# Optimization experiments

Measured on AMD Instinct MI355X. Metric: run time of the kernel, lower is better.

Reference implementation:

```python
import jax, jax.numpy as jnp
import numpy as np

B, M, DM = 8, 1024, 1024
H, DH, R = 16, 64, 32
DFF, R1, R2, RO = 4096, 512, 512, 512
EPS = 1e-12


def layernorm(x, g, b):
    mu = jnp.mean(x, axis=-1, keepdims=True)
    var = jnp.mean(jnp.square(x - mu), axis=-1, keepdims=True)
    return (x - mu) * jax.lax.rsqrt(var + EPS) * g + b


def setup_inputs() -> dict:
    key = jax.random.key(0)
    ks = jax.random.split(key, 24)
    s = lambda *sh: 1.0 / np.sqrt(sh[-2] if len(sh) > 1 else sh[-1])
    d = {}
    d['x'] = jax.random.normal(ks[0], (B, M, DM), jnp.float32)
    d['mask'] = jnp.zeros((B, M), jnp.float32)  # additive attention mask
    # per-head low-rank QKV factors: P:(H,DM,R), V:(H,R,DH), b:(H,DH)
    for i, nm in enumerate(['q', 'k', 'v']):
        d['P' + nm] = jax.random.normal(ks[1 + 3 * i], (H, DM, R), jnp.float32) * 0.02
        d['V' + nm] = jax.random.normal(ks[2 + 3 * i], (H, R, DH), jnp.float32) * 0.02
        d['b' + nm] = jnp.zeros((H, DH), jnp.float32)
    # attention output projection (low-rank) + LN1
    d['Uo'] = jax.random.normal(ks[10], (DM, RO), jnp.float32) * 0.02
    d['Vo'] = jax.random.normal(ks[11], (RO, DM), jnp.float32) * 0.02
    d['bo_attn'] = jnp.zeros((DM,), jnp.float32)
    d['g1'] = jnp.ones((DM,), jnp.float32)
    d['beta1'] = jnp.zeros((DM,), jnp.float32)
    # FFN low-rank factors + LN2
    d['U1'] = jax.random.normal(ks[12], (DM, R1), jnp.float32) * 0.02
    d['V1'] = jax.random.normal(ks[13], (R1, DFF), jnp.float32) * 0.02
    d['b1'] = jnp.zeros((DFF,), jnp.float32)
    d['U2'] = jax.random.normal(ks[14], (DFF, R2), jnp.float32) * 0.02
    d['V2'] = jax.random.normal(ks[15], (R2, DM), jnp.float32) * 0.02
    d['b2'] = jnp.zeros((DM,), jnp.float32)
    d['g2'] = jnp.ones((DM,), jnp.float32)
    d['beta2'] = jnp.zeros((DM,), jnp.float32)
    return d


def reference(x, mask, Pq, Vq, bq, Pk, Vk, bk, Pv, Vv, bv,
              Uo, Vo, bo_attn, g1, beta1,
              U1, V1, b1, U2, V2, b2, g2, beta2):
    # low-rank Q/K/V: x @ P -> (B,H,M,R), then @ V -> (B,H,M,DH), + bias
    def qkv(P, V, b):
        tmp = jnp.einsum('bmd,hdr->bhmr', x, P)
        return jnp.einsum('bhmr,hre->bhme', tmp, V) + b[None, :, None, :]

    Q = qkv(Pq, Vq, bq)
    K = qkv(Pk, Vk, bk)
    V = qkv(Pv, Vv, bv)
    scale = 1.0 / jnp.sqrt(jnp.asarray(DH, x.dtype))
    scores = jnp.einsum('bhme,bhne->bhmn', Q, K) * scale
    scores = scores + mask[:, None, None, :]  # additive mask broadcast over heads/queries
    probs = jax.nn.softmax(scores, axis=-1)
    attn = jnp.einsum('bhmn,bhne->bhme', probs, V)  # (B,H,M,DH)
    attn = attn.transpose(0, 2, 1, 3).reshape(attn.shape[0], attn.shape[2], -1)  # (B,M,DM)
    x1 = layernorm(x + (attn @ Uo) @ Vo + bo_attn, g1, beta1)
    # FFN: GELU((x1 @ U1) @ V1 + b1) @ U2 @ V2 + b2 (flashsvd_ffn semantics)
    mid = x1 @ U1
    hidden = jax.nn.gelu(mid @ V1 + b1, approximate=False)
    y = (hidden @ U2) @ V2 + b2
    return layernorm(x1 + y, g2, beta2)
```

## Files before the change

### kernel.cpp

```cpp
#include <hip/hip_runtime.h>
#include <hip/hip_bf16.h>
#include <math.h>

typedef unsigned short u16;
typedef unsigned int u32;
typedef __attribute__((ext_vector_type(8))) short bf16x8;
typedef __attribute__((ext_vector_type(4))) float f32x4;
typedef __attribute__((ext_vector_type(2))) unsigned int u32x2;
typedef __attribute__((ext_vector_type(4))) unsigned int u32x4;

#define B_ 8
#define M_ 1024
#define DM_ 1024
#define H_ 16
#define DH_ 64
#define NR_ 8192

__device__ __forceinline__ u16 f2bf(float f) {
    unsigned u = __float_as_uint(f);
    u += 0x7FFFu + ((u >> 16) & 1u);
    return (u16)(u >> 16);
}

__device__ __forceinline__ void gload16(const void* g, void* l) {
    __builtin_amdgcn_global_load_lds(
        (const __attribute__((address_space(1))) void*)g,
        (__attribute__((address_space(3))) void*)l, 16, 0, 0);
}

__device__ __forceinline__ u32 lds_addr(const void* p) {
    return (u32)(uintptr_t)(const __attribute__((address_space(3))) void*)p;
}

__device__ void conv_dev(const float* __restrict__ in, u16* __restrict__ out,
                         int bid, int tid) {
#pragma unroll
    for (int j = 0; j < 4; ++j) {
        int i = bid * 4096 + j * 1024 + tid * 4;
        float4 v = *reinterpret_cast<const float4*>(in + i);
        unsigned long long p = (unsigned long long)f2bf(v.x)
                             | ((unsigned long long)f2bf(v.y) << 16)
                             | ((unsigned long long)f2bf(v.z) << 32)
                             | ((unsigned long long)f2bf(v.w) << 48);
        *reinterpret_cast<unsigned long long*>(out + i) = p;
    }
}

__device__ void prep_p_dev(const float* __restrict__ P, u16* __restrict__ Pt,
                           int h, int kc, int tid, float* sm) {
    float (*Ps)[33] = (float(*)[33])sm;
#pragma unroll
    for (int i = 0; i < 16; ++i) {
        int e = tid + i * 256;
        int kk = e >> 5, r = e & 31;
        Ps[kk][r] = P[(size_t)h * 32768 + (size_t)(kc + kk) * 32 + r];
    }
    __syncthreads();
#pragma unroll
    for (int i = 0; i < 16; ++i) {
        int e = tid + i * 256;
        int r = e >> 7, k = e & 127;
        Pt[(size_t)(h * 32 + r) * 1024 + kc + k] = f2bf(Ps[k][r]);
    }
}

__device__ void prep_f_dev(const float* __restrict__ V, u16* __restrict__ Ft,
                           int h, int tid, float* sm) {
    float (*Vs)[65] = (float(*)[65])sm;
#pragma unroll
    for (int i = 0; i < 8; ++i) {
        int e = tid + i * 256;
        int r = e >> 6, c = e & 63;
        Vs[r][c] = V[(size_t)h * 2048 + r * 64 + c];
    }
    __syncthreads();
#pragma unroll
    for (int i = 0; i < 8; ++i) {
        int idx = tid + i * 256;
        int e = idx >> 5, r = idx & 31;
        Ft[(size_t)h * 2560 + e * 40 + r] = f2bf(Vs[r][e]);
    }
}

__device__ void transp_dev(const float* __restrict__ in, u16* __restrict__ out,
                           int R, int C, int bx, int by, int tid, float* sm) {
    float (*t)[65] = (float(*)[65])sm;
    const int rb = by * 64, cb = bx * 64;
#pragma unroll
    for (int i = 0; i < 16; ++i) {
        int e = tid + i * 256;
        int r = e >> 6, c = e & 63;
        t[r][c] = in[(size_t)(rb + r) * C + cb + c];
    }
    __syncthreads();
#pragma unroll
    for (int i = 0; i < 16; ++i) {
        int e = tid + i * 256;
        int r = e >> 6, c = e & 63;
        out[(size_t)(cb + r) * R + rb + c] = f2bf(t[c][r]);
    }
}

__global__ __launch_bounds__(256) void prep_all(
    const float* __restrict__ x,
    const float* __restrict__ Pq, const float* __restrict__ Pk, const float* __restrict__ Pv,
    const float* __restrict__ Vq, const float* __restrict__ Vk, const float* __restrict__ Vv,
    const float* __restrict__ Uo, const float* __restrict__ Vo,
    const float* __restrict__ U1, const float* __restrict__ V1,
    const float* __restrict__ U2, const float* __restrict__ V2,
    u16* __restrict__ Xb, u16* __restrict__ Pt,
    u16* __restrict__ Ftq, u16* __restrict__ Ftk, u16* __restrict__ Ftv,
    u16* __restrict__ Uot, u16* __restrict__ Vot,
    u16* __restrict__ U1t, u16* __restrict__ V1t,
    u16* __restrict__ U2t, u16* __restrict__ V2t) {
    __shared__ float smem[4224];
    const int bid = blockIdx.x, tid = threadIdx.x;
    if (bid < 2048) {
        conv_dev(x, Xb, bid, tid);
    } else if (bid < 2432) {
        int t = bid - 2048, which = t >> 7, tt = t & 127;
        const float* P = which == 0 ? Pq : (which == 1 ? Pk : Pv);
        prep_p_dev(P, Pt + (size_t)which * 524288, tt >> 3, (tt & 7) * 128, tid, smem);
    } else if (bid < 2480) {
        int t = bid - 2432, which = t >> 4;
        const float* V = which == 0 ? Vq : (which == 1 ? Vk : Vv);
        u16* F = which == 0 ? Ftq : (which == 1 ? Ftk : Ftv);
        prep_f_dev(V, F, t & 15, tid, smem);
    } else if (bid < 2608) {
        int t = bid - 2480;
        transp_dev(Uo, Uot, 1024, 512, t & 7, t >> 3, tid, smem);
    } else if (bid < 2736) {
        int t = bid - 2608;
        transp_dev(Vo, Vot, 512, 1024, t & 15, t >> 4, tid, smem);
    } else if (bid < 2864) {
        int t = bid - 2736;
        transp_dev(U1, U1t, 1024, 512, t & 7, t >> 3, tid, smem);
    } else if (bid < 3376) {
        int t = bid - 2864;
        transp_dev(V1, V1t, 512, 4096, t & 63, t >> 6, tid, smem);
    } else if (bid < 3888) {
        int t = bid - 3376;
        transp_dev(U2, U2t, 4096, 512, t & 7, t >> 3, tid, smem);
    } else {
        int t = bid - 3888;
        transp_dev(V2, V2t, 512, 1024, t & 15, t >> 4, tid, smem);
    }
}

template <int EPI, int NF>
__global__ __launch_bounds__(256) void gemm_bf16(const u16* __restrict__ A,
                                                 const u16* __restrict__ Bt,
                                                 const float* __restrict__ bias,
                                                 void* __restrict__ Cout,
                                                 int K, int N) {
    constexpr int BN = NF * 32;
    __shared__ u16 As[128 * 64];
    __shared__ u16 Bs[BN * 64];
    const int tid = threadIdx.x;
    const int lane = tid & 63, wv = tid >> 6;

    const int NX = gridDim.x;
    const int flat = blockIdx.x + blockIdx.y * NX;
    const int q = (NX * gridDim.y) >> 3;
    const int nid = (flat & 7) * q + (flat >> 3);
    const int row0 = (nid / NX) * 128, col0 = (nid % NX) * BN;

    const int frow = lane & 15, fk8 = lane >> 4;
    const int wm = (wv >> 1) * 64, wn = (wv & 1) * (BN / 2);

    f32x4 acc[4][NF];
    const f32x4 z4 = {0.f, 0.f, 0.f, 0.f};
#pragma unroll
    for (int i = 0; i < 4; ++i)
#pragma unroll
        for (int j = 0; j < NF; ++j) acc[i][j] = z4;

    for (int k0 = 0; k0 < K; k0 += 64) {
#pragma unroll
        for (int i = 0; i < 4; ++i) {
            int rr = (i * 4 + wv) * 8 + (lane >> 3);
            int cc = ((lane & 7) ^ (rr & 7)) * 8;
            gload16(A + (size_t)(row0 + rr) * K + k0 + cc,
                    (char*)As + (i * 4 + wv) * 1024);
        }
#pragma unroll
        for (int i = 0; i < NF; ++i) {
            int rr = (i * 4 + wv) * 8 + (lane >> 3);
            int cc = ((lane & 7) ^ (rr & 7)) * 8;
            gload16(Bt + (size_t)(col0 + rr) * K + k0 + cc,
                    (char*)Bs + (i * 4 + wv) * 1024);
        }
        asm volatile("s_waitcnt vmcnt(0)" ::: "memory");
        __syncthreads();
#pragma unroll
        for (int kf = 0; kf < 2; ++kf) {
            bf16x8 af[4], bfr[NF];
#pragma unroll
            for (int mf = 0; mf < 4; ++mf) {
                int r = wm + mf * 16 + frow;
                int c16 = (kf * 4 + fk8) ^ (r & 7);
                af[mf] = *reinterpret_cast<const bf16x8*>((char*)As + r * 128 + c16 * 16);
            }
#pragma unroll
            for (int nf = 0; nf < NF; ++nf) {
                int r = wn + nf * 16 + frow;
                int c16 = (kf * 4 + fk8) ^ (r & 7);
                bfr[nf] = *reinterpret_cast<const bf16x8*>((char*)Bs + r * 128 + c16 * 16);
            }
#pragma unroll
            for (int mf = 0; mf < 4; ++mf)
#pragma unroll
                for (int nf = 0; nf < NF; ++nf)
                    acc[mf][nf] = __builtin_amdgcn_mfma_f32_16x16x32_bf16(
                        af[mf], bfr[nf], acc[mf][nf], 0, 0, 0);
        }
        __syncthreads();
    }

    const int orow = fk8 * 4, ocol = frow;
#pragma unroll
    for (int mf = 0; mf < 4; ++mf)
#pragma unroll
        for (int nf = 0; nf < NF; ++nf)
#pragma unroll
            for (int j = 0; j < 4; ++j) {
                int row = row0 + wm + mf * 16 + orow + j;
                int col = col0 + wn + nf * 16 + ocol;
                float v = acc[mf][nf][j];
                if (EPI == 2) {
                    v += bias[col];
                    v = 0.5f * v * (1.f + erff(v * 0.70710678118f));
                    ((u16*)Cout)[(size_t)row * N + col] = f2bf(v);
                } else if (EPI == 3) {
                    ((float*)Cout)[(size_t)row * N + col] = v;
                } else {
                    ((u16*)Cout)[(size_t)row * N + col] = f2bf(v);
                }
            }
}

__global__ __launch_bounds__(256) void gemm_qkv(const u16* __restrict__ A,
                                                const u16* __restrict__ Bt,
                                                const u16* __restrict__ Ftq,
                                                const u16* __restrict__ Ftk,
                                                const u16* __restrict__ Ftv,
                                                const float* __restrict__ bq,
                                                const float* __restrict__ bk,
                                                const float* __restrict__ bv,
                                                u16* __restrict__ Qo,
                                                u16* __restrict__ Ko,
                                                u16* __restrict__ Vo) {
    const int K = 1024;
    __shared__ u16 As[128 * 64];
    __shared__ u16 Bs[128 * 64];
    const int tid = threadIdx.x;
    const int lane = tid & 63, wv = tid >> 6;

    const int NX = gridDim.x;
    const int flat = blockIdx.x + blockIdx.y * NX;
    const int q = (NX * gridDim.y) >> 3;
    const int nid = (flat & 7) * q + (flat >> 3);
    const int row0 = (nid / NX) * 128, col0 = (nid % NX) * 128;

    const int frow = lane & 15, fk8 = lane >> 4;
    const int wm = (wv >> 1) * 64, wn = (wv & 1) * 64;

    f32x4 acc[4][4];
    const f32x4 z4 = {0.f, 0.f, 0.f, 0.f};
#pragma unroll
    for (int i = 0; i < 4; ++i)
#pragma unroll
        for (int j = 0; j < 4; ++j) acc[i][j] = z4;

    for (int k0 = 0; k0 < K; k0 += 64) {
#pragma unroll
        for (int i = 0; i < 4; ++i) {
            int rr = (i * 4 + wv) * 8 + (lane >> 3);
            int cc = ((lane & 7) ^ (rr & 7)) * 8;
            gload16(A + (size_t)(row0 + rr) * K + k0 + cc,
                    (char*)As + (i * 4 + wv) * 1024);
            gload16(Bt + (size_t)(col0 + rr) * K + k0 + cc,
                    (char*)Bs + (i * 4 + wv) * 1024);
        }
        asm volatile("s_waitcnt vmcnt(0)" ::: "memory");
        __syncthreads();
#pragma unroll
        for (int kf = 0; kf < 2; ++kf) {
            bf16x8 af[4], bfr[4];
#pragma unroll
            for (int mf = 0; mf < 4; ++mf) {
                int r = wm + mf * 16 + frow;
                int c16 = (kf * 4 + fk8) ^ (r & 7);
                af[mf] = *reinterpret_cast<const bf16x8*>((char*)As + r * 128 + c16 * 16);
            }
#pragma unroll
            for (int nf = 0; nf < 4; ++nf) {
                int r = wn + nf * 16 + frow;
                int c16 = (kf * 4 + fk8) ^ (r & 7);
                bfr[nf] = *reinterpret_cast<const bf16x8*>((char*)Bs + r * 128 + c16 * 16);
            }
#pragma unroll
            for (int mf = 0; mf < 4; ++mf)
#pragma unroll
                for (int nf = 0; nf < 4; ++nf)
                    acc[mf][nf] = __builtin_amdgcn_mfma_f32_16x16x32_bf16(
                        af[mf], bfr[nf], acc[mf][nf], 0, 0, 0);
        }
        __syncthreads();
    }

    u16* preg = (wv < 2) ? As + wv * 4096 : Bs + (wv - 2) * 4096;
#pragma unroll
    for (int mf = 0; mf < 4; ++mf)
#pragma unroll
        for (int nf = 0; nf < 4; ++nf)
#pragma unroll
            for (int j = 0; j < 4; ++j) {
                int r = mf * 16 + fk8 * 4 + j;
                int c = nf * 16 + frow;
                int byte = r * 128 + (((c >> 3) ^ (r & 7)) * 16) + (c & 7) * 2;
                *(u16*)((char*)preg + byte) = f2bf(acc[mf][nf][j]);
            }
    __syncthreads();

    const int f = col0 >> 9;
    const u16* Ft = f == 0 ? Ftq : (f == 1 ? Ftk : Ftv);
    const float* bias = f == 0 ? bq : (f == 1 ? bk : bv);
    u16* outp = f == 0 ? Qo : (f == 1 ? Ko : Vo);
    const int h0 = (((col0 & 511) + wn) >> 5);

#pragma unroll
    for (int hh = 0; hh < 2; ++hh) {
        const int h = h0 + hh;
        const u16* ftb = Ft + (size_t)h * 2560;
        bf16x8 bf2[4];
#pragma unroll
        for (int ef = 0; ef < 4; ++ef) {
            int e = ef * 16 + frow;
            bf2[ef] = *reinterpret_cast<const bf16x8*>(ftb + e * 40 + fk8 * 8);
        }
#pragma unroll
        for (int mf = 0; mf < 4; ++mf) {
            int r = mf * 16 + frow;
            bf16x8 af = *reinterpret_cast<const bf16x8*>(
                (char*)preg + r * 128 + (((hh * 4 + fk8) ^ (r & 7)) * 16));
#pragma unroll
            for (int ef = 0; ef < 4; ++ef) {
                f32x4 o = __builtin_amdgcn_mfma_f32_16x16x32_bf16(af, bf2[ef], z4, 0, 0, 0);
                int e = ef * 16 + frow;
                float bv_ = bias[h * 64 + e];
#pragma unroll
                for (int j = 0; j < 4; ++j) {
                    int row = row0 + wm + mf * 16 + fk8 * 4 + j;
                    int bb = row >> 10, m = row & 1023;
                    outp[(((size_t)(bb * 16 + h) << 10) + m) * 64 + e] = f2bf(o[j] + bv_);
                }
            }
        }
    }
}

__global__ __launch_bounds__(256) void gemm_db(const u16* __restrict__ A,
                                               const u16* __restrict__ Bt,
                                               u16* __restrict__ Cout,
                                               int K, int N) {
    __shared__ u16 As[2][128 * 64];
    __shared__ u16 Bs[2][64 * 64];
    const int tid = threadIdx.x;
    const int lane = tid & 63, wv = tid >> 6;

    const int NX = gridDim.x;
    const int flat = blockIdx.x + blockIdx.y * NX;
    const int q = (NX * gridDim.y) >> 3;
    const int nid = (flat & 7) * q + (flat >> 3);
    const int row0 = (nid / NX) * 128, col0 = (nid % NX) * 64;

    const int frow = lane & 15, fk8 = lane >> 4;
    const int wm = (wv >> 1) * 64, wn = (wv & 1) * 32;

    f32x4 acc[4][2];
    const f32x4 z4 = {0.f, 0.f, 0.f, 0.f};
#pragma unroll
    for (int i = 0; i < 4; ++i) {
        acc[i][0] = z4;
        acc[i][1] = z4;
    }

    const int srr = (lane >> 3);
    const int scc = (lane & 7);

#pragma unroll
    for (int i = 0; i < 4; ++i) {
        int rr = (i * 4 + wv) * 8 + srr;
        int cc = (scc ^ (rr & 7)) * 8;
        gload16(A + (size_t)(row0 + rr) * K + cc, (char*)&As[0][0] + (i * 4 + wv) * 1024);
    }
#pragma unroll
    for (int i = 0; i < 2; ++i) {
        int rr = (i * 4 + wv) * 8 + srr;
        int cc = (scc ^ (rr & 7)) * 8;
        gload16(Bt + (size_t)(col0 + rr) * K + cc, (char*)&Bs[0][0] + (i * 4 + wv) * 1024);
    }

    int cur = 0;
    for (int k0 = 0; k0 < K; k0 += 64) {
        __syncthreads();
        if (k0 + 64 < K) {
            int kn = k0 + 64;
#pragma unroll
            for (int i = 0; i < 4; ++i) {
                int rr = (i * 4 + wv) * 8 + srr;
                int cc = (scc ^ (rr & 7)) * 8;
                gload16(A + (size_t)(row0 + rr) * K + kn + cc,
                        (char*)&As[cur ^ 1][0] + (i * 4 + wv) * 1024);
            }
#pragma unroll
            for (int i = 0; i < 2; ++i) {
                int rr = (i * 4 + wv) * 8 + srr;
                int cc = (scc ^ (rr & 7)) * 8;
                gload16(Bt + (size_t)(col0 + rr) * K + kn + cc,
                        (char*)&Bs[cur ^ 1][0] + (i * 4 + wv) * 1024);
            }
        }
#pragma unroll
        for (int kf = 0; kf < 2; ++kf) {
            bf16x8 af[4], bfr[2];
#pragma unroll
            for (int mf = 0; mf < 4; ++mf) {
                int r = wm + mf * 16 + frow;
                int c16 = (kf * 4 + fk8) ^ (r & 7);
                af[mf] = *reinterpret_cast<const bf16x8*>((char*)&As[cur][0] + r * 128 + c16 * 16);
            }
#pragma unroll
            for (int nf = 0; nf < 2; ++nf) {
                int r = wn + nf * 16 + frow;
                int c16 = (kf * 4 + fk8) ^ (r & 7);
                bfr[nf] = *reinterpret_cast<const bf16x8*>((char*)&Bs[cur][0] + r * 128 + c16 * 16);
            }
#pragma unroll
            for (int mf = 0; mf < 4; ++mf)
#pragma unroll
                for (int nf = 0; nf < 2; ++nf)
                    acc[mf][nf] = __builtin_amdgcn_mfma_f32_16x16x32_bf16(
                        af[mf], bfr[nf], acc[mf][nf], 0, 0, 0);
        }
        cur ^= 1;
    }

#pragma unroll
    for (int mf = 0; mf < 4; ++mf)
#pragma unroll
        for (int nf = 0; nf < 2; ++nf)
#pragma unroll
            for (int j = 0; j < 4; ++j) {
                int row = row0 + wm + mf * 16 + fk8 * 4 + j;
                int col = col0 + wn + nf * 16 + frow;
                Cout[(size_t)row * N + col] = f2bf(acc[mf][nf][j]);
            }
}

__global__ __launch_bounds__(256) void attn_mfma(const u16* __restrict__ Q,
                                                 const u16* __restrict__ K,
                                                 const u16* __restrict__ V,
                                                 const float* __restrict__ mask,
                                                 u16* __restrict__ O) {
    __shared__ u16 Ks[2][4096];
    __shared__ u16 Vt[2][4096];
    __shared__ u16 Pw[4096];
    const int flat = blockIdx.x;
    const int nid = (flat & 7) * 256 + (flat >> 3);
    const int hb = nid >> 4, qt = nid & 15;
    const int b = hb >> 4, h = hb & 15;
    const int tid = threadIdx.x, lane = tid & 63, wv = tid >> 6;
    const int frow = lane & 15, fk8 = lane >> 4;
    const size_t base = (size_t)hb * 65536;
    const float LOG2E = 1.44269504089f;
    const int srr = lane >> 3, scc = lane & 7;

    int voff[2];
#pragma unroll
    for (int i = 0; i < 2; ++i) {
        int c = (i * 4 + wv) * 64 + lane;
        int kb = c >> 5, db = (c >> 3) & 3, kr = (c >> 1) & 3, hf = c & 1;
        voff[i] = (kb * 4 + kr) * 64 + db * 16 + hf * 8;
    }

#pragma unroll
    for (int i = 0; i < 2; ++i) {
        int rr = (i * 4 + wv) * 8 + srr;
        int cc = (scc ^ (rr & 7)) * 8;
        gload16(Q + base + (size_t)(qt * 64 + rr) * 64 + cc,
                (char*)Pw + (i * 4 + wv) * 1024);
        gload16(K + base + (size_t)rr * 64 + cc,
                (char*)&Ks[0][0] + (i * 4 + wv) * 1024);
    }
#pragma unroll
    for (int i = 0; i < 2; ++i)
        gload16(V + base + voff[i], (char*)&Vt[0][0] + (i * 4 + wv) * 1024);
    asm volatile("s_waitcnt vmcnt(0)" ::: "memory");
    __syncthreads();

    bf16x8 qfrag[2];
#pragma unroll
    for (int kf = 0; kf < 2; ++kf) {
        int qr = wv * 16 + frow;
        int c16 = (kf * 4 + fk8) ^ (qr & 7);
        qfrag[kf] = *reinterpret_cast<const bf16x8*>((char*)Pw + qr * 128 + c16 * 16);
    }

    u32 vta[4];
    {
        u32 vt0 = lds_addr(&Vt[0][0]) + fk8 * 1024 + frow * 2;
#pragma unroll
        for (int nf = 0; nf < 4; ++nf) vta[nf] = vt0 + nf * 128;
    }

    char* pwW = (char*)Pw + wv * 2048 + frow * 128 + (fk8 & 1) * 8;
    char* pwR = (char*)Pw + wv * 2048 + frow * 128;
    const float* mrow = mask + b * M_;

    float m_i = -1e30f, l_i = 0.f;
    const f32x4 z4 = {0.f, 0.f, 0.f, 0.f};
    f32x4 o_acc[4] = {z4, z4, z4, z4};

    int cur = 0;
    for (int kt = 0; kt < 16; ++kt) {
        if (kt < 15) {
            const int nxt = cur ^ 1;
#pragma unroll
            for (int i = 0; i < 2; ++i) {
                int rr = (i * 4 + wv) * 8 + srr;
                int cc = (scc ^ (rr & 7)) * 8;
                gload16(K + base + (kt + 1) * 4096 + (size_t)rr * 64 + cc,
                        (char*)&Ks[nxt][0] + (i * 4 + wv) * 1024);
            }
#pragma unroll
            for (int i = 0; i < 2; ++i)
                gload16(V + base + (kt + 1) * 4096 + voff[i],
                        (char*)&Vt[nxt][0] + (i * 4 + wv) * 1024);
        }

        const char* ksb = (char*)&Ks[cur][0];
        const u32 vbo = (u32)(cur * 8192);

        f32x4 sacc[4] = {z4, z4, z4, z4};
        __builtin_amdgcn_s_setprio(1);
#pragma unroll
        for (int kf = 0; kf < 2; ++kf)
#pragma unroll
            for (int nf = 0; nf < 4; ++nf) {
                int kr = nf * 16 + frow;
                int c16 = (kf * 4 + fk8) ^ (kr & 7);
                bf16x8 ak = *reinterpret_cast<const bf16x8*>(ksb + kr * 128 + c16 * 16);
                sacc[nf] = __builtin_amdgcn_mfma_f32_16x16x32_bf16(ak, qfrag[kf], sacc[nf], 0, 0, 0);
            }
        __builtin_amdgcn_s_setprio(0);

        float tval[4][4];
        float tmax = -1e30f;
#pragma unroll
        for (int nf = 0; nf < 4; ++nf) {
            float4 mk = *reinterpret_cast<const float4*>(mrow + kt * 64 + nf * 16 + fk8 * 4);
            float t0 = fmaf(sacc[nf][0], 0.125f, mk.x);
            float t1 = fmaf(sacc[nf][1], 0.125f, mk.y);
            float t2 = fmaf(sacc[nf][2], 0.125f, mk.z);
            float t3 = fmaf(sacc[nf][3], 0.125f, mk.w);
            tval[nf][0] = t0; tval[nf][1] = t1; tval[nf][2] = t2; tval[nf][3] = t3;
            tmax = fmaxf(tmax, fmaxf(fmaxf(t0, t1), fmaxf(t2, t3)));
        }
        tmax = fmaxf(tmax, __shfl_xor(tmax, 16));
        tmax = fmaxf(tmax, __shfl_xor(tmax, 32));

        if (__any(tmax > m_i + 8.f)) {
            float mnew = fmaxf(m_i, tmax);
            float c = exp2f((m_i - mnew) * LOG2E);
            m_i = mnew;
            l_i *= c;
#pragma unroll
            for (int j = 0; j < 4; ++j) {
                float cj = __shfl(c, fk8 * 4 + j);
#pragma unroll
                for (int nf = 0; nf < 4; ++nf) o_acc[nf][j] *= cj;
            }
        }

        const float ml = m_i * LOG2E;
        float rs = 0.f;
#pragma unroll
        for (int nf = 0; nf < 4; ++nf) {
            float p0 = exp2f(fmaf(tval[nf][0], LOG2E, -ml));
            float p1 = exp2f(fmaf(tval[nf][1], LOG2E, -ml));
            float p2 = exp2f(fmaf(tval[nf][2], LOG2E, -ml));
            float p3 = exp2f(fmaf(tval[nf][3], LOG2E, -ml));
            rs += (p0 + p1) + (p2 + p3);
            u32 w0 = __builtin_amdgcn_perm(__float_as_uint(p1), __float_as_uint(p0), 0x07060302u);
            u32 w1 = __builtin_amdgcn_perm(__float_as_uint(p3), __float_as_uint(p2), 0x07060302u);
            u32x2 wp = {w0, w1};
            *reinterpret_cast<u32x2*>(pwW + (((nf * 2 + (fk8 >> 1)) ^ (frow & 7)) * 16)) = wp;
        }
        rs += __shfl_xor(rs, 16);
        rs += __shfl_xor(rs, 32);
        l_i += rs;

#pragma unroll
        for (int kf = 0; kf < 2; ++kf) {
            bf16x8 ap = *reinterpret_cast<const bf16x8*>(pwR + (((kf * 4 + fk8) ^ (frow & 7)) * 16));
            u32 a0 = vta[0] + vbo, a1 = vta[1] + vbo, a2 = vta[2] + vbo, a3 = vta[3] + vbo;
            u32x2 r0, r1, r2, r3, r4, r5, r6, r7;
            if (kf == 0) {
                asm volatile("ds_read_b64_tr_b16 %0, %1" : "=&v"(r0) : "v"(a0));
                asm volatile("ds_read_b64_tr_b16 %0, %1 offset:512" : "=&v"(r1) : "v"(a0));
                asm volatile("ds_read_b64_tr_b16 %0, %1" : "=&v"(r2) : "v"(a1));
                asm volatile("ds_read_b64_tr_b16 %0, %1 offset:512" : "=&v"(r3) : "v"(a1));
                asm volatile("ds_read_b64_tr_b16 %0, %1" : "=&v"(r4) : "v"(a2));
                asm volatile("ds_read_b64_tr_b16 %0, %1 offset:512" : "=&v"(r5) : "v"(a2));
                asm volatile("ds_read_b64_tr_b16 %0, %1" : "=&v"(r6) : "v"(a3));
                asm volatile("ds_read_b64_tr_b16 %0, %1 offset:512" : "=&v"(r7) : "v"(a3));
            } else {
                asm volatile("ds_read_b64_tr_b16 %0, %1 offset:4096" : "=&v"(r0) : "v"(a0));
                asm volatile("ds_read_b64_tr_b16 %0, %1 offset:4608" : "=&v"(r1) : "v"(a0));
                asm volatile("ds_read_b64_tr_b16 %0, %1 offset:4096" : "=&v"(r2) : "v"(a1));
                asm volatile("ds_read_b64_tr_b16 %0, %1 offset:4608" : "=&v"(r3) : "v"(a1));
                asm volatile("ds_read_b64_tr_b16 %0, %1 offset:4096" : "=&v"(r4) : "v"(a2));
                asm volatile("ds_read_b64_tr_b16 %0, %1 offset:4608" : "=&v"(r5) : "v"(a2));
                asm volatile("ds_read_b64_tr_b16 %0, %1 offset:4096" : "=&v"(r6) : "v"(a3));
                asm volatile("ds_read_b64_tr_b16 %0, %1 offset:4608" : "=&v"(r7) : "v"(a3));
            }
            asm volatile("s_waitcnt lgkmcnt(0)" ::: "memory");
            __builtin_amdgcn_sched_barrier(0);
            __builtin_amdgcn_s_setprio(1);
            {
                u32x4 vv = {r0.x, r0.y, r1.x, r1.y};
                bf16x8 fb; __builtin_memcpy(&fb, &vv, 16);
                o_acc[0] = __builtin_amdgcn_mfma_f32_16x16x32_bf16(ap, fb, o_acc[0], 0, 0, 0);
            }
            {
                u32x4 vv = {r2.x, r2.y, r3.x, r3.y};
                bf16x8 fb; __builtin_memcpy(&fb, &vv, 16);
                o_acc[1] = __builtin_amdgcn_mfma_f32_16x16x32_bf16(ap, fb, o_acc[1], 0, 0, 0);
            }
            {
                u32x4 vv = {r4.x, r4.y, r5.x, r5.y};
                bf16x8 fb; __builtin_memcpy(&fb, &vv, 16);
                o_acc[2] = __builtin_amdgcn_mfma_f32_16x16x32_bf16(ap, fb, o_acc[2], 0, 0, 0);
            }
            {
                u32x4 vv = {r6.x, r6.y, r7.x, r7.y};
                bf16x8 fb; __builtin_memcpy(&fb, &vv, 16);
                o_acc[3] = __builtin_amdgcn_mfma_f32_16x16x32_bf16(ap, fb, o_acc[3], 0, 0, 0);
            }
            __builtin_amdgcn_s_setprio(0);
        }

        asm volatile("s_waitcnt vmcnt(0)" ::: "memory");
        __syncthreads();
        cur ^= 1;
    }

#pragma unroll
    for (int j = 0; j < 4; ++j) {
        float lq = __shfl(l_i, fk8 * 4 + j);
        float inv = 1.f / lq;
        int grow = qt * 64 + wv * 16 + fk8 * 4 + j;
        size_t obase = ((size_t)(b * M_ + grow)) * DM_ + h * 64;
#pragma unroll
        for (int nf = 0; nf < 4; ++nf)
            O[obase + nf * 16 + frow] = f2bf(o_acc[nf][j] * inv);
    }
}

template <bool WBF>
__global__ __launch_bounds__(256) void ln_kernel(const float* __restrict__ y,
                                                 const float* __restrict__ res,
                                                 const float* __restrict__ bias,
                                                 const float* __restrict__ g,
                                                 const float* __restrict__ beta,
                                                 float* __restrict__ outf,
                                                 u16* __restrict__ outb) {
    __shared__ float red[2][4];
    const int row = blockIdx.x, tid = threadIdx.x;
    const size_t base = (size_t)row * 1024 + tid * 4;
    float4 v = *reinterpret_cast<const float4*>(y + base);
    float4 r = *reinterpret_cast<const float4*>(res + base);
    float4 bb = *reinterpret_cast<const float4*>(bias + tid * 4);
    v.x += r.x + bb.x; v.y += r.y + bb.y; v.z += r.z + bb.z; v.w += r.w + bb.w;
    float sum = v.x + v.y + v.z + v.w;
    float sq = v.x * v.x + v.y * v.y + v.z * v.z + v.w * v.w;
#pragma unroll
    for (int off = 32; off; off >>= 1) {
        sum += __shfl_down(sum, off);
        sq += __shfl_down(sq, off);
    }
    if ((tid & 63) == 0) { red[0][tid >> 6] = sum; red[1][tid >> 6] = sq; }
    __syncthreads();
    sum = red[0][0] + red[0][1] + red[0][2] + red[0][3];
    sq = red[1][0] + red[1][1] + red[1][2] + red[1][3];
    float mu = sum * (1.f / 1024.f);
    float var = sq * (1.f / 1024.f) - mu * mu;
    float rstd = rsqrtf(var + 1e-12f);
    float4 gg = *reinterpret_cast<const float4*>(g + tid * 4);
    float4 be = *reinterpret_cast<const float4*>(beta + tid * 4);
    float4 o;
    o.x = (v.x - mu) * rstd * gg.x + be.x;
    o.y = (v.y - mu) * rstd * gg.y + be.y;
    o.z = (v.z - mu) * rstd * gg.z + be.z;
    o.w = (v.w - mu) * rstd * gg.w + be.w;
    *reinterpret_cast<float4*>(outf + base) = o;
    if (WBF) {
        unsigned long long p = (unsigned long long)f2bf(o.x)
                             | ((unsigned long long)f2bf(o.y) << 16)
                             | ((unsigned long long)f2bf(o.z) << 32)
                             | ((unsigned long long)f2bf(o.w) << 48);
        *reinterpret_cast<unsigned long long*>(outb + base) = p;
    }
}

extern "C" void kernel_launch(void* const* d_in, const int* in_sizes, int n_in,
                              void* d_out, int out_size, void* d_ws, size_t ws_size,
                              hipStream_t stream) {
    const float* x    = (const float*)d_in[0];
    const float* mask = (const float*)d_in[1];
    const float* Pq   = (const float*)d_in[2];
    const float* Vq   = (const float*)d_in[3];
    const float* bq   = (const float*)d_in[4];
    const float* Pk   = (const float*)d_in[5];
    const float* Vk   = (const float*)d_in[6];
    const float* bk   = (const float*)d_in[7];
    const float* Pv   = (const float*)d_in[8];
    const float* Vv   = (const float*)d_in[9];
    const float* bv   = (const float*)d_in[10];
    const float* Uo   = (const float*)d_in[11];
    const float* Vo   = (const float*)d_in[12];
    const float* bo   = (const float*)d_in[13];
    const float* g1   = (const float*)d_in[14];
    const float* be1  = (const float*)d_in[15];
    const float* U1   = (const float*)d_in[16];
    const float* V1   = (const float*)d_in[17];
    const float* b1   = (const float*)d_in[18];
    const float* U2   = (const float*)d_in[19];
    const float* V2   = (const float*)d_in[20];
    const float* b2   = (const float*)d_in[21];
    const float* g2   = (const float*)d_in[22];
    const float* be2  = (const float*)d_in[23];
    float* out = (float*)d_out;

    const size_t MB = 1048576;
    char* ws = (char*)d_ws;
    u16* Pt  = (u16*)(ws + 0);
    u16* Ftq = (u16*)(ws + 3 * MB);
    u16* Ftk = (u16*)(ws + 3 * MB + 131072);
    u16* Ftv = (u16*)(ws + 3 * MB + 262144);
    u16* Uot = (u16*)(ws + 4 * MB);
    u16* Vot = (u16*)(ws + 5 * MB);
    u16* U1t = (u16*)(ws + 6 * MB);
    u16* V1t = (u16*)(ws + 7 * MB);
    u16* U2t = (u16*)(ws + 11 * MB);
    u16* V2t = (u16*)(ws + 15 * MB);
    u16* Xb  = (u16*)(ws + 16 * MB);
    u16* Qb  = (u16*)(ws + 56 * MB);
    u16* Kb  = (u16*)(ws + 72 * MB);
    u16* Vb  = (u16*)(ws + 88 * MB);
    u16* Ob  = (u16*)(ws + 104 * MB);
    u16* Hb  = (u16*)(ws + 32 * MB);
    float* Yf = (float*)(ws + 56 * MB);
    u16* Tb  = (u16*)(ws + 96 * MB);
    float* X1f = (float*)(ws + 120 * MB);

    prep_all<<<4016, 256, 0, stream>>>(x, Pq, Pk, Pv, Vq, Vk, Vv,
                                       Uo, Vo, U1, V1, U2, V2,
                                       Xb, Pt, Ftq, Ftk, Ftv,
                                       Uot, Vot, U1t, V1t, U2t, V2t);

    gemm_qkv<<<dim3(12, 64), 256, 0, stream>>>(Xb, Pt, Ftq, Ftk, Ftv,
                                               bq, bk, bv, Qb, Kb, Vb);

    attn_mfma<<<2048, 256, 0, stream>>>(Qb, Kb, Vb, mask, Ob);

    gemm_db<<<dim3(8, 64), 256, 0, stream>>>(Ob, Uot, Tb, 1024, 512);
    gemm_bf16<3, 4><<<dim3(8, 64), 256, 0, stream>>>(Tb, Vot, nullptr, Yf, 512, 1024);
    ln_kernel<true><<<8192, 256, 0, stream>>>(Yf, x, bo, g1, be1, X1f, Xb);

    gemm_db<<<dim3(8, 64), 256, 0, stream>>>(Xb, U1t, Tb, 1024, 512);
    gemm_bf16<2, 4><<<dim3(32, 64), 256, 0, stream>>>(Tb, V1t, b1, Hb, 512, 4096);
    gemm_db<<<dim3(8, 64), 256, 0, stream>>>(Hb, U2t, Tb, 4096, 512);
    gemm_bf16<3, 4><<<dim3(8, 64), 256, 0, stream>>>(Tb, V2t, nullptr, Yf, 512, 1024);
    ln_kernel<false><<<8192, 256, 0, stream>>>(Yf, X1f, b2, g2, be2, out, nullptr);
}
```

Baseline: 335.5 us.

## Keep P in registers, single-buffer K, pad V tile to raise attention occupancy

The attention kernel stops staging softmax probabilities through LDS. It packs the bf16 P values directly into MFMA A-operand registers by permuting the V key order to match. K becomes single-buffered, V is padded to avoid bank conflicts, Q is staged in the V buffer, and launch bounds ask for 8 blocks per CU. The intent is less LDS traffic and footprint so more blocks fit per CU. The cost is an extra barrier per iteration and less overlap between the K prefetch and compute.

```diff
diff --git a/kernel.cpp b/kernel.cpp
--- a/kernel.cpp
+++ b/kernel.cpp
@@ -459,14 +459,13 @@
             }
 }
 
-__global__ __launch_bounds__(256) void attn_mfma(const u16* __restrict__ Q,
-                                                 const u16* __restrict__ K,
-                                                 const u16* __restrict__ V,
-                                                 const float* __restrict__ mask,
-                                                 u16* __restrict__ O) {
-    __shared__ u16 Ks[2][4096];
-    __shared__ u16 Vt[2][4096];
-    __shared__ u16 Pw[4096];
+__global__ __launch_bounds__(256, 8) void attn_mfma(const u16* __restrict__ Q,
+                                                    const u16* __restrict__ K,
+                                                    const u16* __restrict__ V,
+                                                    const float* __restrict__ mask,
+                                                    u16* __restrict__ O) {
+    __shared__ u16 Ks[4096];
+    __shared__ u16 Vt[8448];
     const int flat = blockIdx.x;
     const int nid = (flat & 7) * 256 + (flat >> 3);
     const int hb = nid >> 4, qt = nid & 15;
@@ -480,9 +479,10 @@
     int voff[2];
 #pragma unroll
     for (int i = 0; i < 2; ++i) {
-        int c = (i * 4 + wv) * 64 + lane;
-        int kb = c >> 5, db = (c >> 3) & 3, kr = (c >> 1) & 3, hf = c & 1;
-        voff[i] = (kb * 4 + kr) * 64 + db * 16 + hf * 8;
+        int r = i * 4 + wv;
+        int keyp = (2 * (r >> 2) + (lane >> 5)) * 16 + (r & 3) * 4 + ((lane >> 1) & 3);
+        int d = ((lane >> 3) & 3) * 16 + (lane & 1) * 8;
+        voff[i] = keyp * 64 + d;
     }
 
 #pragma unroll
@@ -490,33 +490,31 @@
         int rr = (i * 4 + wv) * 8 + srr;
         int cc = (scc ^ (rr & 7)) * 8;
         gload16(Q + base + (size_t)(qt * 64 + rr) * 64 + cc,
-                (char*)Pw + (i * 4 + wv) * 1024);
-        gload16(K + base + (size_t)rr * 64 + cc,
-                (char*)&Ks[0][0] + (i * 4 + wv) * 1024);
-    }
-#pragma unroll
-    for (int i = 0; i < 2; ++i)
-        gload16(V + base + voff[i], (char*)&Vt[0][0] + (i * 4 + wv) * 1024);
+                (char*)Vt + (i * 4 + wv) * 1024);
+    }
     asm volatile("s_waitcnt vmcnt(0)" ::: "memory");
     __syncthreads();
-
     bf16x8 qfrag[2];
 #pragma unroll
     for (int kf = 0; kf < 2; ++kf) {
         int qr = wv * 16 + frow;
         int c16 = (kf * 4 + fk8) ^ (qr & 7);
-        qfrag[kf] = *reinterpret_cast<const bf16x8*>((char*)Pw + qr * 128 + c16 * 16);
-    }
-
-    u32 vta[4];
-    {
-        u32 vt0 = lds_addr(&Vt[0][0]) + fk8 * 1024 + frow * 2;
-#pragma unroll
-        for (int nf = 0; nf < 4; ++nf) vta[nf] = vt0 + nf * 128;
-    }
-
-    char* pwW = (char*)Pw + wv * 2048 + frow * 128 + (fk8 & 1) * 8;
-    char* pwR = (char*)Pw + wv * 2048 + frow * 128;
+        qfrag[kf] = *reinterpret_cast<const bf16x8*>((char*)Vt + qr * 128 + c16 * 16);
+    }
+    __syncthreads();
+#pragma unroll
+    for (int i = 0; i < 2; ++i) {
+        int rr = (i * 4 + wv) * 8 + srr;
+        int cc = (scc ^ (rr & 7)) * 8;
+        gload16(K + base + (size_t)rr * 64 + cc, (char*)Ks + (i * 4 + wv) * 1024);
+    }
+#pragma unroll
+    for (int i = 0; i < 2; ++i)
+        gload16(V + base + voff[i], (char*)Vt + (i * 4 + wv) * 1056);
+    asm volatile("s_waitcnt vmcnt(0)" ::: "memory");
+    __syncthreads();
+
+    const u32 plbase = lds_addr(Vt) + fk8 * 1056 + frow * 2;
     const float* mrow = mask + b * M_;
 
     float m_i = -1e30f, l_i = 0.f;
@@ -525,6 +523,20 @@
 
     int cur = 0;
     for (int kt = 0; kt < 16; ++kt) {
+        f32x4 sacc[4] = {z4, z4, z4, z4};
+        __builtin_amdgcn_s_setprio(1);
+#pragma unroll
+        for (int kf = 0; kf < 2; ++kf)
+#pragma unroll
+            for (int nf = 0; nf < 4; ++nf) {
+                int kr = nf * 16 + frow;
+                int c16 = (kf * 4 + fk8) ^ (kr & 7);
+                bf16x8 ak = *reinterpret_cast<const bf16x8*>((char*)Ks + kr * 128 + c16 * 16);
+                sacc[nf] = __builtin_amdgcn_mfma_f32_16x16x32_bf16(ak, qfrag[kf], sacc[nf], 0, 0, 0);
+            }
+        __builtin_amdgcn_s_setprio(0);
+        __syncthreads();
+
         if (kt < 15) {
             const int nxt = cur ^ 1;
 #pragma unroll
@@ -532,29 +544,13 @@
                 int rr = (i * 4 + wv) * 8 + srr;
                 int cc = (scc ^ (rr & 7)) * 8;
                 gload16(K + base + (kt + 1) * 4096 + (size_t)rr * 64 + cc,
-                        (char*)&Ks[nxt][0] + (i * 4 + wv) * 1024);
+                        (char*)Ks + (i * 4 + wv) * 1024);
             }
 #pragma unroll
             for (int i = 0; i < 2; ++i)
                 gload16(V + base + (kt + 1) * 4096 + voff[i],
-                        (char*)&Vt[nxt][0] + (i * 4 + wv) * 1024);
-        }
-
-        const char* ksb = (char*)&Ks[cur][0];
-        const u32 vbo = (u32)(cur * 8192);
-
-        f32x4 sacc[4] = {z4, z4, z4, z4};
-        __builtin_amdgcn_s_setprio(1);
-#pragma unroll
-        for (int kf = 0; kf < 2; ++kf)
-#pragma unroll
-            for (int nf = 0; nf < 4; ++nf) {
-                int kr = nf * 16 + frow;
-                int c16 = (kf * 4 + fk8) ^ (kr & 7);
-                bf16x8 ak = *reinterpret_cast<const bf16x8*>(ksb + kr * 128 + c16 * 16);
-                sacc[nf] = __builtin_amdgcn_mfma_f32_16x16x32_bf16(ak, qfrag[kf], sacc[nf], 0, 0, 0);
-            }
-        __builtin_amdgcn_s_setprio(0);
+                        (char*)Vt + nxt * 8448 + (i * 4 + wv) * 1056);
+        }
 
         float tval[4][4];
         float tmax = -1e30f;
@@ -586,6 +582,7 @@
 
         const float ml = m_i * LOG2E;
         float rs = 0.f;
+        u32 w0[4], w1[4];
 #pragma unroll
         for (int nf = 0; nf < 4; ++nf) {
             float p0 = exp2f(fmaf(tval[nf][0], LOG2E, -ml));
@@ -593,39 +590,29 @@
             float p2 = exp2f(fmaf(tval[nf][2], LOG2E, -ml));
             float p3 = exp2f(fmaf(tval[nf][3], LOG2E, -ml));
             rs += (p0 + p1) + (p2 + p3);
-            u32 w0 = __builtin_amdgcn_perm(__float_as_uint(p1), __float_as_uint(p0), 0x07060302u);
-            u32 w1 = __builtin_amdgcn_perm(__float_as_uint(p3), __float_as_uint(p2), 0x07060302u);
-            u32x2 wp = {w0, w1};
-            *reinterpret_cast<u32x2*>(pwW + (((nf * 2 + (fk8 >> 1)) ^ (frow & 7)) * 16)) = wp;
+            w0[nf] = __builtin_amdgcn_perm(__float_as_uint(p1), __float_as_uint(p0), 0x07060302u);
+            w1[nf] = __builtin_amdgcn_perm(__float_as_uint(p3), __float_as_uint(p2), 0x07060302u);
         }
         rs += __shfl_xor(rs, 16);
         rs += __shfl_xor(rs, 32);
         l_i += rs;
 
+        const u32 vb = plbase + (u32)(cur * 8448);
 #pragma unroll
         for (int kf = 0; kf < 2; ++kf) {
-            bf16x8 ap = *reinterpret_cast<const bf16x8*>(pwR + (((kf * 4 + fk8) ^ (frow & 7)) * 16));
-            u32 a0 = vta[0] + vbo, a1 = vta[1] + vbo, a2 = vta[2] + vbo, a3 = vta[3] + vbo;
+            u32x4 apv = {w0[kf * 2], w1[kf * 2], w0[kf * 2 + 1], w1[kf * 2 + 1]};
+            bf16x8 ap;
+            __builtin_memcpy(&ap, &apv, 16);
+            u32 a = vb + (u32)(kf * 4224);
             u32x2 r0, r1, r2, r3, r4, r5, r6, r7;
-            if (kf == 0) {
-                asm volatile("ds_read_b64_tr_b16 %0, %1" : "=&v"(r0) : "v"(a0));
-                asm volatile("ds_read_b64_tr_b16 %0, %1 offset:512" : "=&v"(r1) : "v"(a0));
-                asm volatile("ds_read_b64_tr_b16 %0, %1" : "=&v"(r2) : "v"(a1));
-                asm volatile("ds_read_b64_tr_b16 %0, %1 offset:512" : "=&v"(r3) : "v"(a1));
-                asm volatile("ds_read_b64_tr_b16 %0, %1" : "=&v"(r4) : "v"(a2));
-                asm volatile("ds_read_b64_tr_b16 %0, %1 offset:512" : "=&v"(r5) : "v"(a2));
-                asm volatile("ds_read_b64_tr_b16 %0, %1" : "=&v"(r6) : "v"(a3));
-                asm volatile("ds_read_b64_tr_b16 %0, %1 offset:512" : "=&v"(r7) : "v"(a3));
-            } else {
-                asm volatile("ds_read_b64_tr_b16 %0, %1 offset:4096" : "=&v"(r0) : "v"(a0));
-                asm volatile("ds_read_b64_tr_b16 %0, %1 offset:4608" : "=&v"(r1) : "v"(a0));
-                asm volatile("ds_read_b64_tr_b16 %0, %1 offset:4096" : "=&v"(r2) : "v"(a1));
-                asm volatile("ds_read_b64_tr_b16 %0, %1 offset:4608" : "=&v"(r3) : "v"(a1));
-                asm volatile("ds_read_b64_tr_b16 %0, %1 offset:4096" : "=&v"(r4) : "v"(a2));
-                asm volatile("ds_read_b64_tr_b16 %0, %1 offset:4608" : "=&v"(r5) : "v"(a2));
-                asm volatile("ds_read_b64_tr_b16 %0, %1 offset:4096" : "=&v"(r6) : "v"(a3));
-                asm volatile("ds_read_b64_tr_b16 %0, %1 offset:4608" : "=&v"(r7) : "v"(a3));
-            }
+            asm volatile("ds_read_b64_tr_b16 %0, %1" : "=&v"(r0) : "v"(a));
+            asm volatile("ds_read_b64_tr_b16 %0, %1 offset:512" : "=&v"(r1) : "v"(a));
+            asm volatile("ds_read_b64_tr_b16 %0, %1 offset:128" : "=&v"(r2) : "v"(a));
+            asm volatile("ds_read_b64_tr_b16 %0, %1 offset:640" : "=&v"(r3) : "v"(a));
+            asm volatile("ds_read_b64_tr_b16 %0, %1 offset:256" : "=&v"(r4) : "v"(a));
+            asm volatile("ds_read_b64_tr_b16 %0, %1 offset:768" : "=&v"(r5) : "v"(a));
+            asm volatile("ds_read_b64_tr_b16 %0, %1 offset:384" : "=&v"(r6) : "v"(a));
+            asm volatile("ds_read_b64_tr_b16 %0, %1 offset:896" : "=&v"(r7) : "v"(a));
             asm volatile("s_waitcnt lgkmcnt(0)" ::: "memory");
             __builtin_amdgcn_sched_barrier(0);
             __builtin_amdgcn_s_setprio(1);
```

Result: no change. 338.8 us (+1.0%).
